# Performance work log

Measured on AMD Instinct MI355X. Metric: run time of the kernel, lower is better.

The kernel has to match this reference:

```python
import jax, jax.numpy as jnp
import numpy as np

N = 8192
E = 262144
NFEAT, NHID, NCLASS = 128, 256, 16


def setup_inputs() -> dict:
    key = jax.random.key(0)
    k = jax.random.split(key, 6)
    x = jax.random.normal(k[0], (N, NFEAT), dtype=jnp.float32)
    edge_index = jax.random.randint(k[1], (2, E), 0, N, dtype=jnp.int64)
    edge_weight = jax.random.uniform(k[2], (E,), dtype=jnp.float32)
    W1 = jax.random.normal(k[3], (NFEAT, NHID), dtype=jnp.float32) * (1.0 / np.sqrt(NFEAT))
    b1 = jnp.zeros((NHID,), dtype=jnp.float32)
    W2 = jax.random.normal(k[4], (NHID, NCLASS), dtype=jnp.float32) * (1.0 / np.sqrt(NHID))
    b2 = jnp.zeros((NCLASS,), dtype=jnp.float32)
    return {"x": x, "edge_index": edge_index, "edge_weight": edge_weight,
            "W1": W1, "b1": b1, "W2": W2, "b2": b2}


def _norm_adj(edge_index, edge_weight, num_nodes, dtype):
    # dense scatter-add adjacency (adj[row, col] += w), matching the torch code
    adj = jnp.zeros((num_nodes, num_nodes), dtype=dtype)
    adj = adj.at[edge_index[0], edge_index[1]].add(edge_weight)
    adj = adj + jnp.eye(num_nodes, dtype=dtype)  # self loops
    # degree computed under no_grad in the original -> stop_gradient here
    deg = jax.lax.stop_gradient(jnp.sum(adj, axis=1))
    dinv = jnp.where(deg > 0, deg ** -0.5, jnp.zeros_like(deg))  # inf -> 0
    # D^{-1/2} A D^{-1/2} (diag matmuls expressed as broadcasts, same math)
    return dinv[:, None] * adj * dinv[None, :]


def reference(x, edge_index, edge_weight, W1, b1, W2, b2):
    norm_adj = _norm_adj(edge_index, edge_weight, x.shape[0], x.dtype)
    # submodel: 2-layer GCN, relu(A X W1) -> A H W2 -> log_softmax
    h = jax.nn.relu(norm_adj @ (x @ W1) + b1)
    out = norm_adj @ (h @ W2) + b2
    return jax.nn.log_softmax(out, axis=-1)
```

## Files before the change

kernel.cpp:

```cpp
#include <hip/hip_runtime.h>
#include <math.h>

#define N_NODES 8192
#define N_EDGES 262144
#define NFEAT 128
#define NHID 256
#define NCLASS 16
#define ELLS 96


__device__ inline unsigned int f2bf(float f) {
    unsigned int u = __float_as_uint(f);
    u += 0x7fffu + ((u >> 16) & 1u);
    return u >> 16;
}
__device__ inline float bf_lo(unsigned int u) { return __uint_as_float(u << 16); }
__device__ inline float bf_hi(unsigned int u) { return __uint_as_float(u & 0xffff0000u); }

__global__ void zero_kernel(int* __restrict__ p) {
    p[blockIdx.x * 256 + threadIdx.x] = 0;
}

__global__ __launch_bounds__(256) void histscatter_kernel(const int* __restrict__ ei,
                                                          const float* __restrict__ ew,
                                                          int* __restrict__ cnt,
                                                          int2* __restrict__ ell) {
    int e = blockIdx.x * 256 + threadIdx.x;
    int r = ei[e];
    int c = ei[N_EDGES + e];
    float w = ew[e];
    int slot = atomicAdd(&cnt[r], 1);
    ell[r * ELLS + slot] = make_int2(c, __float_as_int(w));
}

__global__ __launch_bounds__(256) void dinvcvt_kernel(const int* __restrict__ cnt,
                                                      const int2* __restrict__ ell,
                                                      const float* __restrict__ x,
                                                      float* __restrict__ dinv,
                                                      uint2* __restrict__ xs) {
    int t = threadIdx.x;
    int lane = t & 31;
    int r = blockIdx.x * 8 + (t >> 5);
    int n = cnt[r];
    float sum = 0.0f;
    for (int base = 0; base < n; base += 32) {
        int idx = base + lane;
        if (idx < n) sum += __int_as_float(ell[r * ELLS + idx].y);
    }
    #pragma unroll
    for (int off = 1; off < 32; off <<= 1) sum += __shfl_xor(sum, off, 32);
    float di = rsqrtf(sum + 1.0f);
    if (lane == 0) dinv[r] = di;
    float4 a = ((const float4*)(x + (size_t)r * NFEAT + lane * 4))[0];
    uint2 o;
    o.x = f2bf(di * a.x) | (f2bf(di * a.y) << 16);
    o.y = f2bf(di * a.z) | (f2bf(di * a.w) << 16);
    xs[r * 32 + lane] = o;
}

__global__ __launch_bounds__(512) void layer12_kernel(const int* __restrict__ cnt,
                                                      const int2* __restrict__ ell,
                                                      const unsigned int* __restrict__ xs1,
                                                      const float* __restrict__ dinv,
                                                      const float* __restrict__ W1,
                                                      const float* __restrict__ b1,
                                                      const float* __restrict__ W2,
                                                      float* __restrict__ V2s) {
    __shared__ float axs[8][NFEAT];
    __shared__ float psum[8][NHID];
    __shared__ float hs[8][NHID + 4];
    __shared__ float part[512];
    int t = threadIdx.x;

    int lane = t & 63;
    int rloc = t >> 6;
    int r = blockIdx.x * 8 + rloc;
    int n = cnt[r];
    float di = dinv[r];
    unsigned int xv = xs1[r * 64 + lane];
    float acc0 = bf_lo(xv), acc1 = bf_hi(xv);
    for (int base = 0; base < n; base += 16) {
        int idx = base + (lane & 15);
        int2 cw = ell[r * ELLS + idx];
        int cc = cw.x & (N_NODES - 1);
        float wl = __int_as_float(cw.y);
        wl = (idx < n) ? wl : 0.0f;
        #pragma unroll
        for (int u = 0; u < 16; ++u) {
            int c = __shfl(cc, u, 16);
            float w = __shfl(wl, u, 16);
            unsigned int v = xs1[c * 64 + lane];
            acc0 += w * bf_lo(v);
            acc1 += w * bf_hi(v);
        }
    }
    ((float2*)&axs[rloc][lane * 2])[0] = make_float2(di * acc0, di * acc1);
    __syncthreads();

    int col = t & 255;
    int kh = t >> 8;
    float hacc[8];
    #pragma unroll
    for (int q = 0; q < 8; ++q) hacc[q] = 0.0f;
    int k0 = kh * 64;
    #pragma unroll 4
    for (int k = k0; k < k0 + 64; ++k) {
        float w = W1[k * NHID + col];
        #pragma unroll
        for (int q = 0; q < 8; ++q) hacc[q] += axs[q][k] * w;
    }
    if (kh == 0) {
        #pragma unroll
        for (int q = 0; q < 8; ++q) psum[q][col] = hacc[q];
    }
    __syncthreads();
    if (kh == 1) {
        float bb = b1[col];
        #pragma unroll
        for (int q = 0; q < 8; ++q) {
            float v = psum[q][col] + hacc[q] + bb;
            hs[q][col] = v > 0.0f ? v : 0.0f;
        }
    }
    __syncthreads();

    int j = t & 15;
    int rq = (t >> 4) & 7;
    int kb = (t >> 7) * 64;
    float p = 0.0f;
    #pragma unroll 8
    for (int k = 0; k < 64; ++k) p += hs[rq][kb + k] * W2[(kb + k) * NCLASS + j];
    part[t] = p;
    __syncthreads();
    if (t < 128) {
        int rg = blockIdx.x * 8 + (t >> 4);
        V2s[rg * NCLASS + (t & 15)] =
            dinv[rg] * (part[t] + part[t + 128] + part[t + 256] + part[t + 384]);
    }
}

__global__ __launch_bounds__(256) void agg2_kernel(const int* __restrict__ cnt,
                                                   const int2* __restrict__ ell,
                                                   const float* __restrict__ V2s,
                                                   const float* __restrict__ dinv,
                                                   const float* __restrict__ b2,
                                                   float* __restrict__ out) {
    int t = threadIdx.x;
    int lane = t & 31;
    int g = lane >> 4;
    int j = lane & 15;
    int r = blockIdx.x * 8 + (t >> 5);
    int n = cnt[r];
    float di = dinv[r];
    float acc = (g == 0) ? V2s[r * NCLASS + j] : 0.0f;
    for (int base = g * 16; base < n; base += 32) {
        int idx = base + j;
        int2 cw = ell[r * ELLS + idx];
        int cc = cw.x & (N_NODES - 1);
        float wl = __int_as_float(cw.y);
        wl = (idx < n) ? wl : 0.0f;
        #pragma unroll
        for (int u = 0; u < 16; ++u) {
            int c = __shfl(cc, u, 16);
            float w = __shfl(wl, u, 16);
            acc += w * V2s[c * NCLASS + j];
        }
    }
    acc += __shfl_xor(acc, 16, 32);
    float v = di * acc + b2[j];
    float mx = v;
    #pragma unroll
    for (int off = 1; off < 16; off <<= 1) mx = fmaxf(mx, __shfl_xor(mx, off));
    float ex = expf(v - mx);
    float ssum = ex;
    #pragma unroll
    for (int off = 1; off < 16; off <<= 1) ssum += __shfl_xor(ssum, off);
    if (g == 0) out[r * NCLASS + j] = v - mx - logf(ssum);
}

extern "C" void kernel_launch(void* const* d_in, const int* in_sizes, int n_in,
                              void* d_out, int out_size, void* d_ws, size_t ws_size,
                              hipStream_t stream) {
    const float* x  = (const float*)d_in[0];
    const int*   ei = (const int*)d_in[1];
    const float* ew = (const float*)d_in[2];
    const float* W1 = (const float*)d_in[3];
    const float* b1 = (const float*)d_in[4];
    const float* W2 = (const float*)d_in[5];
    const float* b2 = (const float*)d_in[6];
    float* out = (float*)d_out;

    const int n = N_NODES;

    char* ws = (char*)d_ws;
    int*   cnt  = (int*)  (ws);
    float* dinv = (float*)(ws + 32768);
    int2*  ell  = (int2*) (ws + 65536);
    float* V2s  = (float*)(ws + 8388608);
    uint2* xs   = (uint2*)(ws + 16777216);

    zero_kernel<<<32, 256, 0, stream>>>(cnt);

    histscatter_kernel<<<N_EDGES / 256, 256, 0, stream>>>(ei, ew, cnt, ell);
    dinvcvt_kernel<<<n / 8, 256, 0, stream>>>(cnt, ell, x, dinv, xs);

    layer12_kernel<<<n / 8, 512, 0, stream>>>(cnt, ell, (const unsigned int*)xs,
                                              dinv, W1, b1, W2, V2s);
    agg2_kernel<<<n / 8, 256, 0, stream>>>(cnt, ell, V2s, dinv, b2, out);
}
```

Baseline: 59.67 us.

## Fold degree computation into edge scatter and apply symmetric normalization per edge

Computes the weighted degree with float atomics inside the edge scatter kernel. The same launch also converts x to bf16 in extra blocks, which removes the separate dinv/convert kernel. The aggregation kernels now stage each row's neighbor list in shared memory with the normalized weight w*dinv[r]*dinv[c] precomputed, replacing the per-lane shuffle broadcasts with LDS reads. The cost is extra gathers of deg[c] in both aggregation kernels, plus float-atomic contention and nondeterministic summation order for the degree.

```diff
diff --git a/kernel.cpp b/kernel.cpp
--- a/kernel.cpp
+++ b/kernel.cpp
@@ -23,49 +23,43 @@
 
 __global__ __launch_bounds__(256) void histscatter_kernel(const int* __restrict__ ei,
                                                           const float* __restrict__ ew,
+                                                          const float* __restrict__ x,
+                                                          float* __restrict__ deg,
                                                           int* __restrict__ cnt,
-                                                          int2* __restrict__ ell) {
-    int e = blockIdx.x * 256 + threadIdx.x;
-    int r = ei[e];
-    int c = ei[N_EDGES + e];
-    float w = ew[e];
-    int slot = atomicAdd(&cnt[r], 1);
-    ell[r * ELLS + slot] = make_int2(c, __float_as_int(w));
-}
-
-__global__ __launch_bounds__(256) void dinvcvt_kernel(const int* __restrict__ cnt,
-                                                      const int2* __restrict__ ell,
-                                                      const float* __restrict__ x,
-                                                      float* __restrict__ dinv,
-                                                      uint2* __restrict__ xs) {
+                                                          int2* __restrict__ ell,
+                                                          uint4* __restrict__ xb4) {
     int t = threadIdx.x;
-    int lane = t & 31;
-    int r = blockIdx.x * 8 + (t >> 5);
-    int n = cnt[r];
-    float sum = 0.0f;
-    for (int base = 0; base < n; base += 32) {
-        int idx = base + lane;
-        if (idx < n) sum += __int_as_float(ell[r * ELLS + idx].y);
-    }
-    #pragma unroll
-    for (int off = 1; off < 32; off <<= 1) sum += __shfl_xor(sum, off, 32);
-    float di = rsqrtf(sum + 1.0f);
-    if (lane == 0) dinv[r] = di;
-    float4 a = ((const float4*)(x + (size_t)r * NFEAT + lane * 4))[0];
-    uint2 o;
-    o.x = f2bf(di * a.x) | (f2bf(di * a.y) << 16);
-    o.y = f2bf(di * a.z) | (f2bf(di * a.w) << 16);
-    xs[r * 32 + lane] = o;
-}
-
-__global__ __launch_bounds__(512) void layer12_kernel(const int* __restrict__ cnt,
+    int b = blockIdx.x;
+    if (b < 1024) {
+        int e = b * 256 + t;
+        int r = ei[e];
+        int c = ei[N_EDGES + e];
+        float w = ew[e];
+        atomicAdd(&deg[r], w);
+        int slot = atomicAdd(&cnt[r], 1);
+        ell[r * ELLS + slot] = make_int2(c, __float_as_int(w));
+    } else {
+        int idx = ((b - 1024) * 256 + t) * 8;
+        float4 a = ((const float4*)(x + idx))[0];
+        float4 c4 = ((const float4*)(x + idx))[1];
+        uint4 o;
+        o.x = f2bf(a.x) | (f2bf(a.y) << 16);
+        o.y = f2bf(a.z) | (f2bf(a.w) << 16);
+        o.z = f2bf(c4.x) | (f2bf(c4.y) << 16);
+        o.w = f2bf(c4.z) | (f2bf(c4.w) << 16);
+        xb4[idx >> 3] = o;
+    }
+}
+
+__global__ __launch_bounds__(512) void layer12_kernel(const float* __restrict__ deg,
+                                                      const int* __restrict__ cnt,
                                                       const int2* __restrict__ ell,
                                                       const unsigned int* __restrict__ xs1,
-                                                      const float* __restrict__ dinv,
                                                       const float* __restrict__ W1,
                                                       const float* __restrict__ b1,
                                                       const float* __restrict__ W2,
-                                                      float* __restrict__ V2s) {
+                                                      float* __restrict__ V2) {
+    __shared__ int2  cwl[8][ELLS];
     __shared__ float axs[8][NFEAT];
     __shared__ float psum[8][NHID];
     __shared__ float hs[8][NHID + 4];
@@ -76,25 +70,30 @@
     int rloc = t >> 6;
     int r = blockIdx.x * 8 + rloc;
     int n = cnt[r];
-    float di = dinv[r];
+    float dr = rsqrtf(deg[r] + 1.0f);
+    int npad = (n + 7) & ~7;
+    for (int idx = lane; idx < npad; idx += 64) {
+        int2 cw = ell[r * ELLS + idx];
+        int c = cw.x & (N_NODES - 1);
+        float w = 0.0f;
+        if (idx < n) w = __int_as_float(cw.y) * dr * rsqrtf(deg[c] + 1.0f);
+        cwl[rloc][idx] = make_int2((idx < n) ? c : 0, __float_as_int(w));
+    }
+
     unsigned int xv = xs1[r * 64 + lane];
-    float acc0 = bf_lo(xv), acc1 = bf_hi(xv);
-    for (int base = 0; base < n; base += 16) {
-        int idx = base + (lane & 15);
-        int2 cw = ell[r * ELLS + idx];
-        int cc = cw.x & (N_NODES - 1);
-        float wl = __int_as_float(cw.y);
-        wl = (idx < n) ? wl : 0.0f;
-        #pragma unroll
-        for (int u = 0; u < 16; ++u) {
-            int c = __shfl(cc, u, 16);
-            float w = __shfl(wl, u, 16);
-            unsigned int v = xs1[c * 64 + lane];
+    float c0 = dr * dr;
+    float acc0 = c0 * bf_lo(xv), acc1 = c0 * bf_hi(xv);
+    for (int base = 0; base < npad; base += 8) {
+        #pragma unroll
+        for (int u = 0; u < 8; ++u) {
+            int2 cw = cwl[rloc][base + u];
+            float w = __int_as_float(cw.y);
+            unsigned int v = xs1[cw.x * 64 + lane];
             acc0 += w * bf_lo(v);
             acc1 += w * bf_hi(v);
         }
     }
-    ((float2*)&axs[rloc][lane * 2])[0] = make_float2(di * acc0, di * acc1);
+    ((float2*)&axs[rloc][lane * 2])[0] = make_float2(acc0, acc1);
     __syncthreads();
 
     int col = t & 255;
@@ -134,40 +133,46 @@
     __syncthreads();
     if (t < 128) {
         int rg = blockIdx.x * 8 + (t >> 4);
-        V2s[rg * NCLASS + (t & 15)] =
-            dinv[rg] * (part[t] + part[t + 128] + part[t + 256] + part[t + 384]);
-    }
-}
-
-__global__ __launch_bounds__(256) void agg2_kernel(const int* __restrict__ cnt,
+        V2[rg * NCLASS + (t & 15)] =
+            part[t] + part[t + 128] + part[t + 256] + part[t + 384];
+    }
+}
+
+__global__ __launch_bounds__(256) void agg2_kernel(const float* __restrict__ deg,
+                                                   const int* __restrict__ cnt,
                                                    const int2* __restrict__ ell,
-                                                   const float* __restrict__ V2s,
-                                                   const float* __restrict__ dinv,
+                                                   const float* __restrict__ V2,
                                                    const float* __restrict__ b2,
                                                    float* __restrict__ out) {
+    __shared__ int2 cwl[8][ELLS];
     int t = threadIdx.x;
     int lane = t & 31;
+    int rloc = t >> 5;
+    int r = blockIdx.x * 8 + rloc;
+    int n = cnt[r];
+    float dr = rsqrtf(deg[r] + 1.0f);
+    int npad = (n + 7) & ~7;
+    for (int idx = lane; idx < npad; idx += 32) {
+        int2 cw = ell[r * ELLS + idx];
+        int c = cw.x & (N_NODES - 1);
+        float w = 0.0f;
+        if (idx < n) w = __int_as_float(cw.y) * dr * rsqrtf(deg[c] + 1.0f);
+        cwl[rloc][idx] = make_int2((idx < n) ? c : 0, __float_as_int(w));
+    }
+
     int g = lane >> 4;
     int j = lane & 15;
-    int r = blockIdx.x * 8 + (t >> 5);
-    int n = cnt[r];
-    float di = dinv[r];
-    float acc = (g == 0) ? V2s[r * NCLASS + j] : 0.0f;
-    for (int base = g * 16; base < n; base += 32) {
-        int idx = base + j;
-        int2 cw = ell[r * ELLS + idx];
-        int cc = cw.x & (N_NODES - 1);
-        float wl = __int_as_float(cw.y);
-        wl = (idx < n) ? wl : 0.0f;
-        #pragma unroll
-        for (int u = 0; u < 16; ++u) {
-            int c = __shfl(cc, u, 16);
-            float w = __shfl(wl, u, 16);
-            acc += w * V2s[c * NCLASS + j];
+    float acc = (g == 0) ? dr * dr * V2[r * NCLASS + j] : 0.0f;
+    for (int base = g * 8; base < npad; base += 16) {
+        #pragma unroll
+        for (int u = 0; u < 8; ++u) {
+            int2 cw = cwl[rloc][base + u];
+            float w = __int_as_float(cw.y);
+            acc += w * V2[cw.x * NCLASS + j];
         }
     }
     acc += __shfl_xor(acc, 16, 32);
-    float v = di * acc + b2[j];
+    float v = acc + b2[j];
     float mx = v;
     #pragma unroll
     for (int off = 1; off < 16; off <<= 1) mx = fmaxf(mx, __shfl_xor(mx, off));
@@ -193,18 +198,17 @@
     const int n = N_NODES;
 
     char* ws = (char*)d_ws;
-    int*   cnt  = (int*)  (ws);
-    float* dinv = (float*)(ws + 32768);
+    float* deg  = (float*)(ws);
+    int*   cnt  = (int*)  (ws + 32768);
     int2*  ell  = (int2*) (ws + 65536);
-    float* V2s  = (float*)(ws + 8388608);
-    uint2* xs   = (uint2*)(ws + 16777216);
-
-    zero_kernel<<<32, 256, 0, stream>>>(cnt);
-
-    histscatter_kernel<<<N_EDGES / 256, 256, 0, stream>>>(ei, ew, cnt, ell);
-    dinvcvt_kernel<<<n / 8, 256, 0, stream>>>(cnt, ell, x, dinv, xs);
-
-    layer12_kernel<<<n / 8, 512, 0, stream>>>(cnt, ell, (const unsigned int*)xs,
-                                              dinv, W1, b1, W2, V2s);
-    agg2_kernel<<<n / 8, 256, 0, stream>>>(cnt, ell, V2s, dinv, b2, out);
-}
+    float* V2   = (float*)(ws + 8388608);
+    uint4* xs   = (uint4*)(ws + 16777216);
+
+    zero_kernel<<<64, 256, 0, stream>>>((int*)ws);
+
+    histscatter_kernel<<<1536, 256, 0, stream>>>(ei, ew, x, deg, cnt, ell, xs);
+
+    layer12_kernel<<<n / 8, 512, 0, stream>>>(deg, cnt, ell, (const unsigned int*)xs,
+                                              W1, b1, W2, V2);
+    agg2_kernel<<<n / 8, 256, 0, stream>>>(deg, cnt, ell, V2, b2, out);
+}
```

Result: slower. 66.11 us (+10.8%).
